# Performance work log

Hardware: AMD Instinct MI355X
Metric: run time of the kernel (lower is better)

The kernel has to match this reference:

```python
import jax, jax.numpy as jnp
import numpy as np

D_MODEL = 512
N_HEADS = 8
BLOCK = 512
D_HEAD = D_MODEL // N_HEADS
SCALE = D_HEAD ** -0.5


def _linear_params(key, d_in, d_out):
    kw, kb = jax.random.split(key)
    bound = 1.0 / np.sqrt(d_in)
    w = jax.random.uniform(kw, (d_in, d_out), jnp.float32, -bound, bound)
    b = jax.random.uniform(kb, (d_out,), jnp.float32, -bound, bound)
    return w, b


def setup_inputs() -> dict:
    key = jax.random.key(0)
    keys = jax.random.split(key, 10)
    x = jax.random.normal(keys[0], (4, 8192, D_MODEL), jnp.float32)
    names = ["lq", "lk", "lv", "lo", "gq", "gk", "gv", "go"]
    inp = {"x": x}
    for i, n in enumerate(names):
        w, b = _linear_params(keys[1 + i], D_MODEL, D_MODEL)
        inp[n + "_w"] = w
        inp[n + "_b"] = b
    gw, gb = _linear_params(keys[9], 2 * D_MODEL, D_MODEL)
    inp["gate_w"] = gw
    inp["gate_b"] = gb
    return inp


def _attend(q, k, v):
    # q,k,v: (..., L, H, Dh) -> (..., L, H, Dh)
    scores = jnp.einsum("...qhd,...khd->...hqk", q, k) * SCALE
    probs = jax.nn.softmax(scores, axis=-1)
    return jnp.einsum("...hqk,...khd->...qhd", probs, v)


def reference(x, lq_w, lq_b, lk_w, lk_b, lv_w, lv_b, lo_w, lo_b,
              gq_w, gq_b, gk_w, gk_b, gv_w, gv_b, go_w, go_b,
              gate_w, gate_b):
    B, S, D = x.shape
    nb = S // BLOCK
    xb = x.reshape(B, nb, BLOCK, D)

    def heads(t, L_axes):
        return t.reshape(t.shape[:-1] + (N_HEADS, D_HEAD))

    # block-local attention (all blocks batched)
    Q = heads(xb @ lq_w + lq_b, None)  # (B, nb, bs, H, Dh)
    K = heads(xb @ lk_w + lk_b, None)
    V = heads(xb @ lv_w + lv_b, None)
    loc = _attend(Q, K, V).reshape(B, nb, BLOCK, D)
    local_out = (loc @ lo_w + lo_b).reshape(B, S, D)

    # pooled block summaries: AdaptiveAvgPool1d(1) == mean over block length
    pooled = xb.mean(axis=2)  # (B, nb, D)
    Qg = heads(pooled @ gq_w + gq_b, None)  # (B, nb, H, Dh)
    Kg = heads(pooled @ gk_w + gk_b, None)
    Vg = heads(pooled @ gv_w + gv_b, None)
    glob = _attend(Qg, Kg, Vg).reshape(B, nb, D)
    glob = glob @ go_w + go_b  # (B, nb, D)

    # broadcast each block summary to its tokens
    global_out = jnp.repeat(glob, BLOCK, axis=1)  # (B, S, D)

    gate_in = jnp.concatenate([local_out, global_out], axis=-1)
    gate = jax.nn.sigmoid(gate_in @ gate_w + gate_b)
    return gate * local_out + (1.0 - gate) * global_out
```

## Files before the change

### kernel.cpp

```cpp
#include <hip/hip_runtime.h>
#include <math.h>

typedef unsigned short u16;
typedef short s16;
typedef u16 u16x8 __attribute__((ext_vector_type(8)));
typedef u16 u16x4 __attribute__((ext_vector_type(4)));
typedef s16 s16x8 __attribute__((ext_vector_type(8)));
typedef float f32x4 __attribute__((ext_vector_type(4)));
typedef unsigned u32x4 __attribute__((ext_vector_type(4)));

__device__ __forceinline__ float b2f(u16 u) { return __uint_as_float(((unsigned)u) << 16); }
__device__ __forceinline__ u16 f2b(float f) {
  unsigned x = __float_as_uint(f);
  unsigned r = x + 0x7fffu + ((x >> 16) & 1u);
  return (u16)(r >> 16);
}
__device__ __forceinline__ unsigned cvtpk(float a, float b) {
  unsigned r;
  asm("v_cvt_pk_bf16_f32 %0, %1, %2" : "=v"(r) : "v"(a), "v"(b));
  return r;
}
union PkH { u32x4 w; s16x8 h; };
union Pk2 { unsigned w[2]; u16x4 h; };

#define SCALE 0.125f
#define SCLG2E 0.1803368801111137f
#define DM 512
#define NTOK 32768

typedef __attribute__((address_space(1))) unsigned int as1_u32;
typedef __attribute__((address_space(3))) unsigned int as3_u32;
__device__ __forceinline__ void gl2lds16(const u16* g, u16* s) {
  __builtin_amdgcn_global_load_lds((as1_u32*)g, (as3_u32*)s, 16, 0, 0);
}

__global__ __launch_bounds__(256)
void conv_psum(const float* __restrict__ X, u16* __restrict__ Xb,
               float* __restrict__ Psum)
{
  __shared__ float ps[4][512];
  const int tid = threadIdx.x;
  const int c8 = (tid & 63) * 8;
  const int rg = tid >> 6;
  const size_t tok0 = (size_t)blockIdx.x * 64;
  f32x4 s0 = {0.f, 0.f, 0.f, 0.f}, s1 = {0.f, 0.f, 0.f, 0.f};
  for (int it = 0; it < 16; ++it) {
    const size_t tok = tok0 + it * 4 + rg;
    const float* xp = X + tok * DM + c8;
    f32x4 a = *(const f32x4*)xp;
    f32x4 b = *(const f32x4*)(xp + 4);
    Pk2 p0, p1;
    p0.w[0] = cvtpk(a[0], a[1]); p0.w[1] = cvtpk(a[2], a[3]);
    p1.w[0] = cvtpk(b[0], b[1]); p1.w[1] = cvtpk(b[2], b[3]);
    *(u16x4*)(Xb + tok * DM + c8)     = p0.h;
    *(u16x4*)(Xb + tok * DM + c8 + 4) = p1.h;
    s0 += a; s1 += b;
  }
  *(f32x4*)&ps[rg][c8]     = s0;
  *(f32x4*)&ps[rg][c8 + 4] = s1;
  __syncthreads();
#pragma unroll
  for (int i = 0; i < 2; ++i) {
    const int col = tid + i * 256;
    Psum[(size_t)blockIdx.x * DM + col] =
        ps[0][col] + ps[1][col] + ps[2][col] + ps[3][col];
  }
}

__global__ __launch_bounds__(256)
void pool_prep(const float* __restrict__ Psum, u16* __restrict__ PB)
{
  const int g = blockIdx.x, tid = threadIdx.x;
#pragma unroll
  for (int i = 0; i < 2; ++i) {
    const int col = tid + i * 256;
    float v = 0.f;
#pragma unroll
    for (int s = 0; s < 8; ++s) v += Psum[(size_t)(g * 8 + s) * DM + col];
    PB[(size_t)g * DM + col] = f2b(v * (1.f / 512.f));
  }
}

__global__ __launch_bounds__(256)
void trans_w(const float* w0, const float* w1, const float* w2, const float* w3,
             const float* w4, const float* w5, const float* w6, const float* w7,
             const float* w8, const float* w9, u16* __restrict__ WT)
{
  __shared__ float t[32][33];
  const int z = blockIdx.z;
  const float* W = (z == 0) ? w0 : (z == 1) ? w1 : (z == 2) ? w2 : (z == 3) ? w3 :
                   (z == 4) ? w4 : (z == 5) ? w5 : (z == 6) ? w6 : (z == 7) ? w7 :
                   (z == 8) ? w8 : w9;
  u16* D = WT + (size_t)z * DM * DM;
  const int tx = threadIdx.x & 31, ty = threadIdx.x >> 5;
  const int n0 = blockIdx.x * 32, k0 = blockIdx.y * 32;
#pragma unroll
  for (int j = 0; j < 4; ++j)
    t[ty + j * 8][tx] = W[(size_t)(k0 + ty + j * 8) * DM + n0 + tx];
  __syncthreads();
#pragma unroll
  for (int j = 0; j < 4; ++j)
    D[(size_t)(n0 + ty + j * 8) * DM + k0 + tx] = f2b(t[tx][ty + j * 8]);
}

__global__ __launch_bounds__(256)
void conv_w(const float* __restrict__ W, u16* __restrict__ D)
{
  const size_t i = ((size_t)blockIdx.x * 256 + threadIdx.x) * 8;
  f32x4 a = *(const f32x4*)(W + i);
  f32x4 b = *(const f32x4*)(W + i + 4);
  Pk2 p0, p1;
  p0.w[0] = cvtpk(a[0], a[1]); p0.w[1] = cvtpk(a[2], a[3]);
  p1.w[0] = cvtpk(b[0], b[1]); p1.w[1] = cvtpk(b[2], b[3]);
  *(u16x4*)(D + i)     = p0.h;
  *(u16x4*)(D + i + 4) = p1.h;
}

__global__ __launch_bounds__(256)
void bc_kernel(const float* __restrict__ go_b, const float* __restrict__ gate_w,
               const float* __restrict__ gate_b, float* __restrict__ bc)
{
  __shared__ float red[8][32];
  const int tid = threadIdx.x;
  const int jj = tid & 31, part = tid >> 5;
  const int j = blockIdx.x * 32 + jj;
  float p = 0.f;
#pragma unroll
  for (int i = 0; i < 64; ++i) {
    const int k = part * 64 + i;
    p = fmaf(go_b[k], gate_w[(size_t)(512 + k) * DM + j], p);
  }
  red[part][jj] = p;
  __syncthreads();
  if (tid < 32) {
    float v = gate_b[blockIdx.x * 32 + tid];
#pragma unroll
    for (int s = 0; s < 8; ++s) v += red[s][tid];
    bc[blockIdx.x * 32 + tid] = v;
  }
}

template<int EPI>
__global__ __launch_bounds__(256)
void gemm_mfma(const u16* __restrict__ A, const u16* __restrict__ Wt,
               const float* __restrict__ bias, u16* __restrict__ Cb,
               float* __restrict__ Cf, float outscale,
               const float* __restrict__ GG)
{
  __shared__ u16 As[2][128 * 32];
  __shared__ u16 Bs[2][128 * 32];
  const int tid = threadIdx.x;
  const int w = tid >> 6, l = tid & 63;
  const int l15 = l & 15, gl = l >> 4;
  const int wm = w >> 1, wn = w & 1;
  const int m0 = blockIdx.y * 128, n0 = blockIdx.x * 128;

  const int rA = w * 16 + (l >> 2);
  const int gsrc = ((l & 3) ^ ((l >> 3) & 3)) * 8;
  const u16* Ag = A  + (size_t)(m0 + rA) * DM + gsrc;
  const u16* Bg = Wt + (size_t)(n0 + rA) * DM + gsrc;

  auto stage = [&](int t, int b) {
    const int k0 = t * 32;
#pragma unroll
    for (int it = 0; it < 2; ++it) {
      gl2lds16(Ag + (size_t)(it * 64) * DM + k0, &As[b][(it * 256 + w * 64) * 8]);
      gl2lds16(Bg + (size_t)(it * 64) * DM + k0, &Bs[b][(it * 256 + w * 64) * 8]);
    }
  };

  f32x4 acc[4][4];
#pragma unroll
  for (int i = 0; i < 4; ++i)
#pragma unroll
    for (int j = 0; j < 4; ++j) acc[i][j] = {0.f, 0.f, 0.f, 0.f};

  const int sw = (l15 >> 1) & 3;
  stage(0, 0);
#pragma unroll
  for (int t = 0; t < 16; ++t) {
    if (t < 15) {
      stage(t + 1, (t + 1) & 1);
      asm volatile("s_waitcnt vmcnt(4)" ::: "memory");
    } else {
      asm volatile("s_waitcnt vmcnt(0)" ::: "memory");
    }
    __builtin_amdgcn_s_barrier();
    __builtin_amdgcn_sched_barrier(0);
    const int b = t & 1;
    s16x8 af[4], bfr[4];
#pragma unroll
    for (int f = 0; f < 4; ++f) {
      af[f]  = *(const s16x8*)&As[b][(wm * 64 + f * 16 + l15) * 32 + (gl ^ sw) * 8];
      bfr[f] = *(const s16x8*)&Bs[b][(wn * 64 + f * 16 + l15) * 32 + (gl ^ sw) * 8];
    }
#pragma unroll
    for (int fm = 0; fm < 4; ++fm)
#pragma unroll
      for (int fn = 0; fn < 4; ++fn) {
        if (EPI == 2)
          acc[fm][fn] = __builtin_amdgcn_mfma_f32_16x16x32_bf16(
              af[fm], bfr[fn], acc[fm][fn], 0, 0, 0);
        else
          acc[fm][fn] = __builtin_amdgcn_mfma_f32_16x16x32_bf16(
              bfr[fn], af[fm], acc[fm][fn], 0, 0, 0);
      }
    __builtin_amdgcn_s_barrier();
  }

  if (EPI == 2) {
#pragma unroll
    for (int fn = 0; fn < 4; ++fn) {
      const int n = n0 + wn * 64 + fn * 16 + l15;
      const float bn = bias[n];
      const int d = n & 63, ghn = n >> 6;
#pragma unroll
      for (int fm = 0; fm < 4; ++fm) {
        const int m = m0 + wm * 64 + fm * 16 + gl * 4;
        const int f = (m & 63) >> 4;
        const int pos = ((f >> 1) << 5) | (gl << 3) | ((f & 1) << 2);
        Pk2 p;
        p.w[0] = cvtpk(acc[fm][fn][0] + bn, acc[fm][fn][1] + bn);
        p.w[1] = cvtpk(acc[fm][fn][2] + bn, acc[fm][fn][3] + bn);
        *(u16x4*)(Cb + ((size_t)(((m >> 9) * 8 + ghn) * 64 + d)) * 512
                     + ((m & 511) >> 6) * 64 + pos) = p.h;
      }
    }
  } else {
#pragma unroll
    for (int fm = 0; fm < 4; ++fm) {
      const int m = m0 + wm * 64 + fm * 16 + l15;
      const int brow = m >> 9;
#pragma unroll
      for (int fn = 0; fn < 4; ++fn) {
        const int nb = n0 + wn * 64 + fn * 16 + gl * 4;
        if (EPI == 0) {
          f32x4 b4 = *(const f32x4*)&bias[nb];
          f32x4 v = (acc[fm][fn] + b4) * outscale;
          Pk2 p;
          p.w[0] = cvtpk(v[0], v[1]);
          p.w[1] = cvtpk(v[2], v[3]);
          *(u16x4*)(Cb + (size_t)m * DM + nb) = p.h;
        } else if (EPI == 3) {
          Pk2 p;
          p.w[0] = cvtpk(acc[fm][fn][0], acc[fm][fn][1]);
          p.w[1] = cvtpk(acc[fm][fn][2], acc[fm][fn][3]);
          *(u16x4*)(Cb + (size_t)m * DM + nb) = p.h;
        } else {
          f32x4 z = acc[fm][fn] + *(const f32x4*)&GG[(size_t)brow * 1024 + 512 + nb];
          u16x4 lo4 = *(const u16x4*)(A + (size_t)m * DM + nb);
          f32x4 go4 = *(const f32x4*)&GG[(size_t)brow * 1024 + nb];
          f32x4 res;
#pragma unroll
          for (int r = 0; r < 4; ++r) {
            float g = 1.f / (1.f + __expf(-z[r]));
            res[r] = g * b2f(lo4[r]) + (1.f - g) * go4[r];
          }
          *(f32x4*)(Cf + (size_t)m * DM + nb) = res;
        }
      }
    }
  }
}

__global__ __launch_bounds__(256)
void gemm64(const u16* __restrict__ A,
            const u16* B0, const u16* B1, const u16* B2,
            const float* b0, const float* b1, const float* b2,
            float* __restrict__ Out, int ldo)
{
  __shared__ u16 As[2][64 * 64];
  __shared__ u16 Bs[2][128 * 64];
  const int tid = threadIdx.x;
  const int w = tid >> 6, l = tid & 63;
  const int l15 = l & 15, gl = l >> 4;
  const int bx = blockIdx.x;
  const int grp = bx >> 2;
  const u16* Bt = ((grp == 0) ? B0 : (grp == 1) ? B1 : B2)
                  + (size_t)(bx & 3) * 128 * DM;
  const float* bias = (grp == 0) ? b0 : (grp == 1) ? b1 : b2;

  const int srow = l >> 3;
  const int scol = ((l & 7) ^ (srow & 7)) * 8;
  const u16* Ag = A  + (size_t)(w * 16 + srow) * DM + scol;
  const u16* Bg = Bt + (size_t)(w * 32 + srow) * DM + scol;

  auto stage = [&](int t, int b) {
    const int k0 = t * 64;
#pragma unroll
    for (int c = 0; c < 2; ++c)
      gl2lds16(Ag + (size_t)(c * 8) * DM + k0, &As[b][(w * 16 + c * 8) * 64]);
#pragma unroll
    for (int c = 0; c < 4; ++c)
      gl2lds16(Bg + (size_t)(c * 8) * DM + k0, &Bs[b][(w * 32 + c * 8) * 64]);
  };

  f32x4 acc[4][2];
#pragma unroll
  for (int i = 0; i < 4; ++i)
#pragma unroll
    for (int j = 0; j < 2; ++j) acc[i][j] = {0.f, 0.f, 0.f, 0.f};

  const int xorv = l15 & 7;
  stage(0, 0);
#pragma unroll
  for (int t = 0; t < 8; ++t) {
    if (t < 7) {
      stage(t + 1, (t + 1) & 1);
      asm volatile("s_waitcnt vmcnt(6)" ::: "memory");
    } else {
      asm volatile("s_waitcnt vmcnt(0)" ::: "memory");
    }
    __builtin_amdgcn_s_barrier();
    __builtin_amdgcn_sched_barrier(0);
    const int b = t & 1;
#pragma unroll
    for (int kd = 0; kd < 2; ++kd) {
      const int go = ((gl + 4 * kd) ^ xorv) * 8;
      s16x8 af[4], bfr[2];
#pragma unroll
      for (int f = 0; f < 4; ++f)
        af[f] = *(const s16x8*)&As[b][(f * 16 + l15) * 64 + go];
#pragma unroll
      for (int f = 0; f < 2; ++f)
        bfr[f] = *(const s16x8*)&Bs[b][(w * 32 + f * 16 + l15) * 64 + go];
#pragma unroll
      for (int fm = 0; fm < 4; ++fm)
#pragma unroll
        for (int fn = 0; fn < 2; ++fn)
          acc[fm][fn] = __builtin_amdgcn_mfma_f32_16x16x32_bf16(
              bfr[fn], af[fm], acc[fm][fn], 0, 0, 0);
    }
    __builtin_amdgcn_s_barrier();
  }

#pragma unroll
  for (int fm = 0; fm < 4; ++fm) {
    const int m = fm * 16 + l15;
#pragma unroll
    for (int fn = 0; fn < 2; ++fn) {
      const int nloc = w * 32 + fn * 16 + gl * 4;
      f32x4 b4 = *(const f32x4*)&bias[(bx & 3) * 128 + nloc];
      *(f32x4*)&Out[(size_t)m * ldo + bx * 128 + nloc] = acc[fm][fn] + b4;
    }
  }
}

__global__ __launch_bounds__(512, 4)
void attn_mfma(const u16* __restrict__ Q, const u16* __restrict__ K,
               const u16* __restrict__ VT, u16* __restrict__ CTX)
{
  __shared__ u16 Ks[64 * 64];
  __shared__ u16 VsT[64 * 64];
  const int tid = threadIdx.x;
  const int w = tid >> 6, l = tid & 63;
  const int l15 = l & 15, gl = l >> 4;
  const int g = blockIdx.x, h = blockIdx.y, qh = blockIdx.z;
  const int t0 = g * 512;
  const int fb = h * 64;
  const int q0 = t0 + qh * 256 + w * 32;
  const u16* VTb = VT + ((size_t)(g * 8 + h) * 64) * 512;

  s16x8 qf[2][2];
#pragma unroll
  for (int fq = 0; fq < 2; ++fq)
#pragma unroll
    for (int kd = 0; kd < 2; ++kd)
      qf[fq][kd] = *(const s16x8*)(Q + (size_t)(q0 + fq * 16 + l15) * DM
                                     + fb + gl * 8 + kd * 32);

  f32x4 o[2][4];
#pragma unroll
  for (int i = 0; i < 2; ++i)
#pragma unroll
    for (int j = 0; j < 4; ++j) o[i][j] = {0.f, 0.f, 0.f, 0.f};
  f32x4 psv[2] = {{0.f,0.f,0.f,0.f}, {0.f,0.f,0.f,0.f}};

  const int srow = tid >> 3;
  const int swg = ((tid & 7) ^ ((tid >> 3) & 7)) * 8;
  const u16* Kg = K + (size_t)(t0 + srow) * DM + fb + swg;
  const u16* Vg = VTb + (size_t)srow * 512 + swg;
  s16x8 kreg = *(const s16x8*)Kg;
  s16x8 vreg = *(const s16x8*)Vg;
  const int sw = l15 & 7;

  for (int kc = 0; kc < 8; ++kc) {
    __syncthreads();
    *(s16x8*)&Ks[tid * 8]  = kreg;
    *(s16x8*)&VsT[tid * 8] = vreg;
    __syncthreads();
    if (kc < 7) {
      kreg = *(const s16x8*)(Kg + (size_t)(kc + 1) * 64 * DM);
      vreg = *(const s16x8*)(Vg + (kc + 1) * 64);
    }

    f32x4 s[4][2];
#pragma unroll
    for (int i = 0; i < 4; ++i)
#pragma unroll
      for (int j = 0; j < 2; ++j) s[i][j] = {0.f, 0.f, 0.f, 0.f};
#pragma unroll
    for (int kd = 0; kd < 2; ++kd) {
      s16x8 kf[4];
#pragma unroll
      for (int fm = 0; fm < 4; ++fm)
        kf[fm] = *(const s16x8*)&Ks[(fm * 16 + l15) * 64 + ((gl + 4 * kd) ^ sw) * 8];
#pragma unroll
      for (int fm = 0; fm < 4; ++fm)
#pragma unroll
        for (int fq = 0; fq < 2; ++fq)
          s[fm][fq] = __builtin_amdgcn_mfma_f32_16x16x32_bf16(
              kf[fm], qf[fq][kd], s[fm][fq], 0, 0, 0);
    }

#pragma unroll
    for (int fq = 0; fq < 2; ++fq)
#pragma unroll
      for (int fm = 0; fm < 4; ++fm) {
#pragma unroll
        for (int r = 0; r < 4; ++r) s[fm][fq][r] = exp2f(s[fm][fq][r]);
        psv[fq] += s[fm][fq];
      }

    PkH pf[2][2];
#pragma unroll
    for (int ka = 0; ka < 2; ++ka)
#pragma unroll
      for (int fq = 0; fq < 2; ++fq) {
        pf[ka][fq].w[0] = cvtpk(s[2 * ka][fq][0], s[2 * ka][fq][1]);
        pf[ka][fq].w[1] = cvtpk(s[2 * ka][fq][2], s[2 * ka][fq][3]);
        pf[ka][fq].w[2] = cvtpk(s[2 * ka + 1][fq][0], s[2 * ka + 1][fq][1]);
        pf[ka][fq].w[3] = cvtpk(s[2 * ka + 1][fq][2], s[2 * ka + 1][fq][3]);
      }

#pragma unroll
    for (int ka = 0; ka < 2; ++ka)
#pragma unroll
      for (int fd = 0; fd < 4; ++fd) {
        s16x8 vf = *(const s16x8*)&VsT[(fd * 16 + l15) * 64 + ((ka * 4 + gl) ^ sw) * 8];
#pragma unroll
        for (int qm = 0; qm < 2; ++qm)
          o[qm][fd] = __builtin_amdgcn_mfma_f32_16x16x32_bf16(
              pf[ka][qm].h, vf, o[qm][fd], 0, 0, 0);
      }
  }

  float l_[2];
#pragma unroll
  for (int fq = 0; fq < 2; ++fq) {
    float t = (psv[fq][0] + psv[fq][1]) + (psv[fq][2] + psv[fq][3]);
    t += __shfl_xor(t, 16);
    t += __shfl_xor(t, 32);
    l_[fq] = t;
  }
#pragma unroll
  for (int qm = 0; qm < 2; ++qm) {
    const float i0 = 1.f / __shfl(l_[qm], gl * 4 + 0);
    const float i1 = 1.f / __shfl(l_[qm], gl * 4 + 1);
    const float i2 = 1.f / __shfl(l_[qm], gl * 4 + 2);
    const float i3 = 1.f / __shfl(l_[qm], gl * 4 + 3);
#pragma unroll
    for (int fd = 0; fd < 4; ++fd) {
      const size_t base = (size_t)(q0 + qm * 16 + gl * 4) * DM + fb + fd * 16 + l15;
      CTX[base]          = f2b(o[qm][fd][0] * i0);
      CTX[base + DM]     = f2b(o[qm][fd][1] * i1);
      CTX[base + 2 * DM] = f2b(o[qm][fd][2] * i2);
      CTX[base + 3 * DM] = f2b(o[qm][fd][3] * i3);
    }
  }
}

__global__ __launch_bounds__(256)
void gattn(const float* __restrict__ QKVg, u16* __restrict__ GlB)
{
  __shared__ float q[16][64], k[16][64], v[16][64];
  __shared__ float sc[16][16];
  const int bh = blockIdx.x;
  const int b = bh >> 3, h = bh & 7;
  const int tid = threadIdx.x;
  for (int idx = tid; idx < 1024; idx += 256) {
    const int n = idx >> 6, d = idx & 63;
    const size_t off = (size_t)(b * 16 + n) * 1536 + h * 64 + d;
    q[n][d] = QKVg[off]; k[n][d] = QKVg[off + 512]; v[n][d] = QKVg[off + 1024];
  }
  __syncthreads();
  {
    const int qq = tid >> 4, kk = tid & 15;
    float s = 0.f;
#pragma unroll
    for (int d = 0; d < 64; ++d) s = fmaf(q[qq][d], k[kk][d], s);
    sc[qq][kk] = s * SCALE;
  }
  __syncthreads();
  if (tid < 16) {
    float mx = -INFINITY;
#pragma unroll
    for (int j = 0; j < 16; ++j) mx = fmaxf(mx, sc[tid][j]);
    float e[16]; float sum = 0.f;
#pragma unroll
    for (int j = 0; j < 16; ++j) { e[j] = __expf(sc[tid][j] - mx); sum += e[j]; }
    const float inv = 1.f / sum;
#pragma unroll
    for (int j = 0; j < 16; ++j) sc[tid][j] = e[j] * inv;
  }
  __syncthreads();
  for (int idx = tid; idx < 1024; idx += 256) {
    const int qq = idx >> 6, d = idx & 63;
    float o = 0.f;
#pragma unroll
    for (int j = 0; j < 16; ++j) o = fmaf(sc[qq][j], v[j][d], o);
    GlB[(size_t)(b * 16 + qq) * DM + h * 64 + d] = f2b(o);
  }
}

extern "C" void kernel_launch(void* const* d_in, const int* in_sizes, int n_in,
                              void* d_out, int out_size, void* d_ws, size_t ws_size,
                              hipStream_t stream)
{
  const float* x      = (const float*)d_in[0];
  const float* lq_w   = (const float*)d_in[1];
  const float* lq_b   = (const float*)d_in[2];
  const float* lk_w   = (const float*)d_in[3];
  const float* lk_b   = (const float*)d_in[4];
  const float* lv_w   = (const float*)d_in[5];
  const float* lv_b   = (const float*)d_in[6];
  const float* lo_w   = (const float*)d_in[7];
  const float* lo_b   = (const float*)d_in[8];
  const float* gq_w   = (const float*)d_in[9];
  const float* gq_b   = (const float*)d_in[10];
  const float* gk_w   = (const float*)d_in[11];
  const float* gk_b   = (const float*)d_in[12];
  const float* gv_w   = (const float*)d_in[13];
  const float* gv_b   = (const float*)d_in[14];
  const float* go_w   = (const float*)d_in[15];
  const float* go_b   = (const float*)d_in[16];
  const float* gate_w = (const float*)d_in[17];
  const float* gate_b = (const float*)d_in[18];
  float* out = (float*)d_out;

  const size_t NE = (size_t)NTOK * DM;
  const size_t DD = (size_t)DM * DM;
  char* ws = (char*)d_ws;
  u16* Qb  = (u16*)ws;
  u16* Kb  = Qb + NE;
  u16* VT  = Kb + NE;
  u16* WT  = VT + NE;
  u16* goD = WT + 10 * DD;
  u16* WcT = goD + DD;
  u16* PB  = WcT + DD;
  u16* GlB = PB + 64 * DM;
  float* scr  = (float*)(GlB + 64 * DM);
  float* Psum = scr;
  float* QKVg = Psum + 512 * DM;
  float* GG   = QKVg + (size_t)64 * 1536;
  float* bc   = GG + (size_t)64 * 1024;
  u16* xb = (u16*)d_out;
  u16* LOCAL = Kb;

  u16* WTq  = WT;
  u16* WTk  = WT + 1 * DD;
  u16* WTv  = WT + 2 * DD;
  u16* WTo  = WT + 3 * DD;
  u16* WTg  = WT + 4 * DD;
  u16* WTgq = WT + 5 * DD;
  u16* WTgk = WT + 6 * DD;
  u16* WTgv = WT + 7 * DD;
  u16* WTgo = WT + 8 * DD;
  u16* WTg2 = WT + 9 * DD;

  conv_psum<<<512, 256, 0, stream>>>(x, xb, Psum);
  trans_w<<<dim3(16, 16, 10), 256, 0, stream>>>(
      lq_w, lk_w, lv_w, lo_w, gate_w, gq_w, gk_w, gv_w, go_w,
      gate_w + DD, WT);
  conv_w<<<128, 256, 0, stream>>>(go_w, goD);
  bc_kernel<<<16, 256, 0, stream>>>(go_b, gate_w, gate_b, bc);
  pool_prep<<<64, 256, 0, stream>>>(Psum, PB);

  const dim3 gg(4, 256), bb(256);
  gemm_mfma<0><<<gg, bb, 0, stream>>>(xb, WTq, lq_b, Qb, nullptr, SCLG2E, nullptr);
  gemm_mfma<0><<<gg, bb, 0, stream>>>(xb, WTk, lk_b, Kb, nullptr, 1.0f, nullptr);
  gemm_mfma<2><<<gg, bb, 0, stream>>>(xb, WTv, lv_b, VT, nullptr, 1.0f, nullptr);
  gemm_mfma<3><<<dim3(4, 4), bb, 0, stream>>>(WTg2, goD, nullptr, WcT, nullptr, 1.0f, nullptr);

  attn_mfma<<<dim3(64, 8, 2), 512, 0, stream>>>(Qb, Kb, VT, Qb );
  gemm_mfma<0><<<gg, bb, 0, stream>>>(Qb , WTo, lo_b, LOCAL, nullptr, 1.0f, nullptr);

  gemm64<<<12, 256, 0, stream>>>(PB, WTgq, WTgk, WTgv, gq_b, gk_b, gv_b, QKVg, 1536);
  gattn<<<32, 256, 0, stream>>>(QKVg, GlB);
  gemm64<<<8, 256, 0, stream>>>(GlB, WTgo, WcT, WcT, go_b, bc, bc, GG, 1024);

  gemm_mfma<1><<<gg, bb, 0, stream>>>(LOCAL, WTg, nullptr, nullptr, out, 1.0f, GG);
}
```

Before: 287.5 us.

## Double GEMM K-tile to 64 with 8-way XOR swizzle and XCD-aware tile mapping

Raises the GEMM k-step from 32 to 64, which halves the number of pipeline iterations and barriers. It changes the LDS layout to 64-wide rows with an 8-way XOR swizzle on both the global-to-LDS copies and the fragment reads. When gridDim.y is 256, it also remaps block indices so that consecutive M-tiles land on the same XCD, which is meant to improve L2 reuse of the A rows. LDS use doubles to 64KB per block, which may lower occupancy.

After: 243.1 us. 1.18x faster.

```diff
diff --git a/kernel.cpp b/kernel.cpp
--- a/kernel.cpp
+++ b/kernel.cpp
@@ -147,25 +147,35 @@
                float* __restrict__ Cf, float outscale,
                const float* __restrict__ GG)
 {
-  __shared__ u16 As[2][128 * 32];
-  __shared__ u16 Bs[2][128 * 32];
+  __shared__ u16 As[2][128 * 64];
+  __shared__ u16 Bs[2][128 * 64];
   const int tid = threadIdx.x;
   const int w = tid >> 6, l = tid & 63;
   const int l15 = l & 15, gl = l >> 4;
   const int wm = w >> 1, wn = w & 1;
-  const int m0 = blockIdx.y * 128, n0 = blockIdx.x * 128;
-
-  const int rA = w * 16 + (l >> 2);
-  const int gsrc = ((l & 3) ^ ((l >> 3) & 3)) * 8;
-  const u16* Ag = A  + (size_t)(m0 + rA) * DM + gsrc;
-  const u16* Bg = Wt + (size_t)(n0 + rA) * DM + gsrc;
+
+  int mt, nt;
+  if (gridDim.y == 256) {
+    const int H = blockIdx.y * 4 + blockIdx.x;
+    const int xcd = H & 7, i = H >> 3;
+    mt = xcd * 32 + (i >> 2);
+    nt = i & 3;
+  } else {
+    mt = blockIdx.y; nt = blockIdx.x;
+  }
+  const int m0 = mt * 128, n0 = nt * 128;
+
+  const int srow = l >> 3;
+  const int scol = ((l & 7) ^ (srow & 7)) * 8;
+  const u16* Ag = A  + (size_t)(m0 + w * 32 + srow) * DM + scol;
+  const u16* Bg = Wt + (size_t)(n0 + w * 32 + srow) * DM + scol;
 
   auto stage = [&](int t, int b) {
-    const int k0 = t * 32;
-#pragma unroll
-    for (int it = 0; it < 2; ++it) {
-      gl2lds16(Ag + (size_t)(it * 64) * DM + k0, &As[b][(it * 256 + w * 64) * 8]);
-      gl2lds16(Bg + (size_t)(it * 64) * DM + k0, &Bs[b][(it * 256 + w * 64) * 8]);
+    const int k0 = t * 64;
+#pragma unroll
+    for (int c = 0; c < 4; ++c) {
+      gl2lds16(Ag + (size_t)(c * 8) * DM + k0, &As[b][(w * 32 + c * 8) * 64]);
+      gl2lds16(Bg + (size_t)(c * 8) * DM + k0, &Bs[b][(w * 32 + c * 8) * 64]);
     }
   };
 
@@ -175,36 +185,40 @@
 #pragma unroll
     for (int j = 0; j < 4; ++j) acc[i][j] = {0.f, 0.f, 0.f, 0.f};
 
-  const int sw = (l15 >> 1) & 3;
+  const int xorv = l15 & 7;
   stage(0, 0);
 #pragma unroll
-  for (int t = 0; t < 16; ++t) {
-    if (t < 15) {
+  for (int t = 0; t < 8; ++t) {
+    if (t < 7) {
       stage(t + 1, (t + 1) & 1);
-      asm volatile("s_waitcnt vmcnt(4)" ::: "memory");
+      asm volatile("s_waitcnt vmcnt(8)" ::: "memory");
     } else {
       asm volatile("s_waitcnt vmcnt(0)" ::: "memory");
     }
     __builtin_amdgcn_s_barrier();
     __builtin_amdgcn_sched_barrier(0);
     const int b = t & 1;
-    s16x8 af[4], bfr[4];
-#pragma unroll
-    for (int f = 0; f < 4; ++f) {
-      af[f]  = *(const s16x8*)&As[b][(wm * 64 + f * 16 + l15) * 32 + (gl ^ sw) * 8];
-      bfr[f] = *(const s16x8*)&Bs[b][(wn * 64 + f * 16 + l15) * 32 + (gl ^ sw) * 8];
-    }
-#pragma unroll
-    for (int fm = 0; fm < 4; ++fm)
-#pragma unroll
-      for (int fn = 0; fn < 4; ++fn) {
-        if (EPI == 2)
-          acc[fm][fn] = __builtin_amdgcn_mfma_f32_16x16x32_bf16(
-              af[fm], bfr[fn], acc[fm][fn], 0, 0, 0);
-        else
-          acc[fm][fn] = __builtin_amdgcn_mfma_f32_16x16x32_bf16(
-              bfr[fn], af[fm], acc[fm][fn], 0, 0, 0);
+#pragma unroll
+    for (int kd = 0; kd < 2; ++kd) {
+      const int go = ((gl + 4 * kd) ^ xorv) * 8;
+      s16x8 af[4], bfr[4];
+#pragma unroll
+      for (int f = 0; f < 4; ++f) {
+        af[f]  = *(const s16x8*)&As[b][(wm * 64 + f * 16 + l15) * 64 + go];
+        bfr[f] = *(const s16x8*)&Bs[b][(wn * 64 + f * 16 + l15) * 64 + go];
       }
+#pragma unroll
+      for (int fm = 0; fm < 4; ++fm)
+#pragma unroll
+        for (int fn = 0; fn < 4; ++fn) {
+          if (EPI == 2)
+            acc[fm][fn] = __builtin_amdgcn_mfma_f32_16x16x32_bf16(
+                af[fm], bfr[fn], acc[fm][fn], 0, 0, 0);
+          else
+            acc[fm][fn] = __builtin_amdgcn_mfma_f32_16x16x32_bf16(
+                bfr[fn], af[fm], acc[fm][fn], 0, 0, 0);
+        }
+    }
     __builtin_amdgcn_s_barrier();
   }
 
```
